# Kernel tuning notes

Measured on AMD Instinct MI355X. Metric: run time of the kernel, lower is better.

Reference implementation:

```python
import jax, jax.numpy as jnp
import numpy as np

BN_EPS = 1e-3  # keras BatchNormalization default epsilon


def batch_norm(x):
    # Fresh keras BatchNorm in training mode: gamma=1, beta=0, batch stats over axis 0
    mean = jnp.mean(x, axis=0, keepdims=True)
    var = jnp.var(x, axis=0, keepdims=True)
    return (x - mean) * jax.lax.rsqrt(var + BN_EPS)


def setup_inputs() -> dict:
    key = jax.random.key(0)
    k1, k2, k3 = jax.random.split(key, 3)
    N, D = 100000, 512
    x1 = jax.random.normal(k1, (N, D), dtype=jnp.float32)
    x2 = jax.random.normal(k2, (N, D), dtype=jnp.float32)
    # glorot_uniform for [D, D] kernel
    limit = np.sqrt(6.0 / (D + D)).astype(np.float32)
    kernel = jax.random.uniform(k3, (D, D), dtype=jnp.float32, minval=-limit, maxval=limit)
    return {"x1": x1, "x2": x2, "kernel": kernel}


def reference(x1, x2, kernel):
    b1 = batch_norm(x1)  # [N, D]
    b2 = batch_norm(x2)  # [N, D]
    gate = jax.nn.relu(jnp.tanh(b1 @ kernel))  # [N, D]; dropout_rate=0 -> no dropout
    out = jnp.tanh(b2 * (1.0 - gate) + b1 * gate)
    return out
```

## Files before the change

kernel.cpp:

```cpp
#include <hip/hip_runtime.h>
#include <hip/hip_fp16.h>
#include <stdint.h>

#define N_ROWS 100000
#define DCOLS 512
#define BN_EPS 1e-3f
#define PB 256

typedef __attribute__((ext_vector_type(8))) _Float16 f16x8;
typedef __attribute__((ext_vector_type(4))) float f32x4;
typedef __attribute__((ext_vector_type(4))) unsigned short u16x4;
typedef __attribute__((ext_vector_type(4))) unsigned int u32x4;

__device__ inline float fast_tanh(float x) {
  float e = __expf(2.0f * x);
  return 1.0f - 2.0f * __builtin_amdgcn_rcpf(e + 1.0f);
}
__device__ inline void gld16(const void* g, void* l) {
  __builtin_amdgcn_global_load_lds(
      (const __attribute__((address_space(1))) void*)g,
      (__attribute__((address_space(3))) void*)l, 16, 0, 0);
}
__device__ inline unsigned int h2u(__half2 h) {
  unsigned int u;
  __builtin_memcpy(&u, &h, 4);
  return u;
}
__device__ inline f16x8 u2f(const u32x4& u) {
  f16x8 h;
  __builtin_memcpy(&h, &u, 16);
  return h;
}

__device__ inline void split8h(const float4& v0, const float4& v1,
                               f16x8& hi8, f16x8& lo8) {
  __half2 h0 = __floats2half2_rn(v0.x, v0.y);
  __half2 h1 = __floats2half2_rn(v0.z, v0.w);
  __half2 h2 = __floats2half2_rn(v1.x, v1.y);
  __half2 h3 = __floats2half2_rn(v1.z, v1.w);
  __half2 l0 = __floats2half2_rn(v0.x - __low2float(h0), v0.y - __high2float(h0));
  __half2 l1 = __floats2half2_rn(v0.z - __low2float(h1), v0.w - __high2float(h1));
  __half2 l2 = __floats2half2_rn(v1.x - __low2float(h2), v1.y - __high2float(h2));
  __half2 l3 = __floats2half2_rn(v1.z - __low2float(h3), v1.w - __high2float(h3));
  u32x4 hi = (u32x4){h2u(h0), h2u(h1), h2u(h2), h2u(h3)};
  u32x4 lo = (u32x4){h2u(l0), h2u(l1), h2u(l2), h2u(l3)};
  hi8 = u2f(hi);
  lo8 = u2f(lo);
}

__global__ __launch_bounds__(256) void k_stats_partial(
    const float* __restrict__ x1, const float* __restrict__ x2,
    float* __restrict__ psum, float* __restrict__ psq) {
  const int CH = (N_ROWS + PB - 1) / PB;
  int bx = blockIdx.x;
  int arr = blockIdx.y;
  const float* x = arr ? x2 : x1;
  int r0 = bx * CH;
  int r1 = min(N_ROWS, r0 + CH);
  int c0 = threadIdx.x * 2;
  float s0 = 0.f, s1 = 0.f, q0 = 0.f, q1 = 0.f;
#pragma unroll 8
  for (int r = r0; r < r1; ++r) {
    float2 v = *(const float2*)(x + (size_t)r * DCOLS + c0);
    s0 += v.x; s1 += v.y;
    q0 += v.x * v.x; q1 += v.y * v.y;
  }
  size_t base = ((size_t)(arr * PB + bx)) * DCOLS + c0;
  psum[base] = s0; psum[base + 1] = s1;
  psq[base]  = q0; psq[base + 1]  = q1;
}

__global__ __launch_bounds__(512) void k_stats_final(
    const float* __restrict__ psum, const float* __restrict__ psq,
    float* __restrict__ stats, float* __restrict__ cvec) {
  int a = blockIdx.x;
  int c = threadIdx.x;
  if (a == 0) cvec[c] = 0.f;
  float sa[8], qa[8];
#pragma unroll
  for (int u = 0; u < 8; ++u) { sa[u] = 0.f; qa[u] = 0.f; }
  for (int b = 0; b < PB; b += 8) {
#pragma unroll
    for (int u = 0; u < 8; ++u) {
      size_t base = ((size_t)(a * PB + b + u)) * DCOLS + c;
      sa[u] += psum[base];
      qa[u] += psq[base];
    }
  }
  float s = ((sa[0]+sa[1])+(sa[2]+sa[3]))+((sa[4]+sa[5])+(sa[6]+sa[7]));
  float q = ((qa[0]+qa[1])+(qa[2]+qa[3]))+((qa[4]+qa[5])+(qa[6]+qa[7]));
  float inv = 1.0f / (float)N_ROWS;
  float mean = s * inv;
  float var = q * inv - mean * mean;
  float scale = rsqrtf(var + BN_EPS);
  stats[a * 1024 + c] = scale;
  stats[a * 1024 + 512 + c] = -mean * scale;
}

__global__ __launch_bounds__(256) void k_prepw(
    const float* __restrict__ wk, const float* __restrict__ stats,
    u32x4* __restrict__ wf, float* __restrict__ cvec) {
  int gid = blockIdx.x * 256 + threadIdx.x;
  int j = gid & 511;
  int kg = gid >> 9;
  int k0 = kg * 8;
  const float* negms1 = stats + 512;
  unsigned short h[8];
  float cacc = 0.f;
#pragma unroll
  for (int u = 0; u < 8; ++u) {
    float wr = wk[(size_t)(k0 + u) * DCOLS + j];
    cacc += negms1[k0 + u] * wr;
    float w = wr * stats[k0 + u];
    __half hh = __float2half_rn(w);
    h[u] = __half_as_ushort(hh);
  }
  atomicAdd(cvec + j, cacc);
  int slice = k0 >> 5;
  int lr = (k0 >> 3) & 3;
  int lane = (lr << 4) | (j & 15);
  int g = j >> 4;
  int idx = slice * 2048 + g * 64 + lane;
  u16x4* ph = (u16x4*)&wf[idx];
  u16x4 h0 = {h[0], h[1], h[2], h[3]};
  u16x4 h1 = {h[4], h[5], h[6], h[7]};
  ph[0] = h0; ph[1] = h1;
}

__global__ __launch_bounds__(512, 4) void k_main(
    const float* __restrict__ x1, const float* __restrict__ x2,
    const float* __restrict__ stats, const float* __restrict__ cvec,
    const u32x4* __restrict__ wf, float* __restrict__ out) {
  __shared__ char smem[32768];

  const int tid = threadIdx.x;
  const int lane = tid & 63;
  const int wv = tid >> 6;
  const int ra = lane & 15;
  const int rq = lane >> 4;

  const int xcd = blockIdx.x & 7;
  const int wgid = xcd * 391 + (blockIdx.x >> 3);
  const int panel = wgid >> 2;
  const int q = wgid & 3;
  const int row0 = panel * 128;
  const int col0 = q * 128;

  int arow = row0 + wv * 16 + ra;
  arow = min(arow, N_ROWS - 1);
  const float* abase = x1 + (size_t)arow * DCOLS + rq * 8;

  const u32x4* bsrc[2];
  int bdst[2];
#pragma unroll
  for (int e = 0; e < 2; ++e) {
    int id = wv * 2 + e;
    int kk = id >> 3, g = id & 7;
    bsrc[e] = wf + (size_t)kk * 2048 + (size_t)(q * 8 + g) * 64 + lane;
    bdst[e] = id * 1024;
  }

  f32x4 acc[8];
#pragma unroll
  for (int g = 0; g < 8; ++g) {
    float cj = cvec[col0 + g * 16 + ra];
    acc[g] = (f32x4){cj, cj, cj, cj};
  }

  float4 av[2][4];

  auto stageB = [&](int s, int buf) {
#pragma unroll
    for (int e = 0; e < 2; ++e)
      gld16(bsrc[e] + (size_t)s * 2 * 2048, smem + buf * 16384 + bdst[e]);
  };
  auto loadA = [&](int s, int pset) {
    const float* p = abase + s * 64;
    av[pset][0] = *(const float4*)(p);
    av[pset][1] = *(const float4*)(p + 4);
    av[pset][2] = *(const float4*)(p + 32);
    av[pset][3] = *(const float4*)(p + 36);
  };

  stageB(0, 0);
  asm volatile("" ::: "memory");
  loadA(0, 0);
  asm volatile("s_waitcnt vmcnt(4)" ::: "memory");
  __builtin_amdgcn_s_barrier();
  __builtin_amdgcn_sched_barrier(0);

#pragma unroll
  for (int s = 0; s < 8; ++s) {
    const int p = s & 1;
    if (s < 7) {
      stageB(s + 1, p ^ 1);
      asm volatile("" ::: "memory");
      loadA(s + 1, p ^ 1);
      __builtin_amdgcn_sched_barrier(0);
    }
#pragma unroll
    for (int kk = 0; kk < 2; ++kk) {
      f16x8 bf[8];
#pragma unroll
      for (int g = 0; g < 8; ++g)
        bf[g] = *(const f16x8*)(smem + p * 16384 + (kk * 8 + g) * 1024 +
                                lane * 16);
      f16x8 ah, al;
      split8h(av[p][kk * 2], av[p][kk * 2 + 1], ah, al);
      __builtin_amdgcn_s_setprio(1);
#pragma unroll
      for (int g = 0; g < 8; ++g)
        acc[g] = __builtin_amdgcn_mfma_f32_16x16x32_f16(ah, bf[g], acc[g],
                                                        0, 0, 0);
#pragma unroll
      for (int g = 0; g < 8; ++g)
        acc[g] = __builtin_amdgcn_mfma_f32_16x16x32_f16(al, bf[g], acc[g],
                                                        0, 0, 0);
      __builtin_amdgcn_s_setprio(0);
    }
    if (s < 7) {
      asm volatile("s_waitcnt vmcnt(4)" ::: "memory");
      __builtin_amdgcn_s_barrier();
      __builtin_amdgcn_sched_barrier(0);
    }
  }

  const float* scale1 = stats;
  const float* negms1 = stats + 512;
  const float* scale2 = stats + 1024;
  const float* negms2 = stats + 1536;

  float s1j[8], n1j[8], s2j[8], n2j[8];
#pragma unroll
  for (int g = 0; g < 8; ++g) {
    int j = col0 + g * 16 + ra;
    s1j[g] = scale1[j]; n1j[g] = negms1[j];
    s2j[g] = scale2[j]; n2j[g] = negms2[j];
  }
#pragma unroll
  for (int r = 0; r < 4; ++r) {
    int n = row0 + wv * 16 + rq * 4 + r;
    if (n < N_ROWS) {
#pragma unroll
      for (int g = 0; g < 8; ++g) {
        int j = col0 + g * 16 + ra;
        float c = acc[g][r];
        float tt = fast_tanh(c);
        float gt = fmaxf(tt, 0.0f);
        size_t idx = (size_t)n * DCOLS + j;
        float b1v = fmaf(x1[idx], s1j[g], n1j[g]);
        float b2v = fmaf(x2[idx], s2j[g], n2j[g]);
        out[idx] = fast_tanh(b2v + gt * (b1v - b2v));
      }
    }
  }
}

extern "C" void kernel_launch(void* const* d_in, const int* in_sizes, int n_in,
                              void* d_out, int out_size, void* d_ws, size_t ws_size,
                              hipStream_t stream) {
  const float* x1 = (const float*)d_in[0];
  const float* x2 = (const float*)d_in[1];
  const float* wk = (const float*)d_in[2];
  float* out = (float*)d_out;
  char* ws = (char*)d_ws;

  if (ws_size < (size_t)(4u << 20)) return;

  float* psum  = (float*)ws;
  float* psq   = (float*)(ws + (1 << 20));
  float* stats = (float*)(ws + (2 << 20));
  float* cvec  = (float*)(ws + (2 << 20) + (160 << 10));
  u32x4* wf    = (u32x4*)(ws + (3 << 20));

  k_stats_partial<<<dim3(PB, 2), 256, 0, stream>>>(x1, x2, psum, psq);
  k_stats_final<<<2, 512, 0, stream>>>(psum, psq, stats, cvec);
  k_prepw<<<128, 256, 0, stream>>>(wk, stats, wf, cvec);

  const int nblocks = 8 * 391;
  k_main<<<nblocks, 512, 0, stream>>>(x1, x2, stats, cvec, wf, out);
}
```

Before: 299.2 us.

## Double K-stage depth to 128 and split A register loads into halves

The GEMM main loop now stages 128 K-values of the fp16 weight tile per step in a 64KB double-buffered LDS region. That halves the number of stages and barriers. A-operand fp32 loads are split into two register halves, so the second half loads while the first half's MFMAs run. The cost is twice the LDS per block, which likely cuts resident blocks per CU below the launch-bounds target of 4. The mid-stage vmcnt(0) wait also blocks on the next B prefetch, which can reduce overlap.

Result: no change. 295.1 us (-1.4%).

```diff
diff --git a/kernel.cpp b/kernel.cpp
--- a/kernel.cpp
+++ b/kernel.cpp
@@ -131,7 +131,7 @@
     const float* __restrict__ x1, const float* __restrict__ x2,
     const float* __restrict__ stats, const float* __restrict__ cvec,
     const u32x4* __restrict__ wf, float* __restrict__ out) {
-  __shared__ char smem[32768];
+  __shared__ char smem[65536];
 
   const int tid = threadIdx.x;
   const int lane = tid & 63;
@@ -150,13 +150,13 @@
   arow = min(arow, N_ROWS - 1);
   const float* abase = x1 + (size_t)arow * DCOLS + rq * 8;
 
-  const u32x4* bsrc[2];
-  int bdst[2];
-#pragma unroll
-  for (int e = 0; e < 2; ++e) {
-    int id = wv * 2 + e;
-    int kk = id >> 3, g = id & 7;
-    bsrc[e] = wf + (size_t)kk * 2048 + (size_t)(q * 8 + g) * 64 + lane;
+  const u32x4* bsrc[4];
+  int bdst[4];
+#pragma unroll
+  for (int e = 0; e < 4; ++e) {
+    int id = wv * 4 + e;
+    int sl = id >> 3, g = id & 7;
+    bsrc[e] = wf + (size_t)sl * 2048 + (size_t)(q * 8 + g) * 64 + lane;
     bdst[e] = id * 1024;
   }
 
@@ -167,46 +167,31 @@
     acc[g] = (f32x4){cj, cj, cj, cj};
   }
 
-  float4 av[2][4];
+  float4 avA[4], avB[4];
 
   auto stageB = [&](int s, int buf) {
 #pragma unroll
-    for (int e = 0; e < 2; ++e)
-      gld16(bsrc[e] + (size_t)s * 2 * 2048, smem + buf * 16384 + bdst[e]);
+    for (int e = 0; e < 4; ++e)
+      gld16(bsrc[e] + (size_t)s * 8192, smem + buf * 32768 + bdst[e]);
   };
-  auto loadA = [&](int s, int pset) {
-    const float* p = abase + s * 64;
-    av[pset][0] = *(const float4*)(p);
-    av[pset][1] = *(const float4*)(p + 4);
-    av[pset][2] = *(const float4*)(p + 32);
-    av[pset][3] = *(const float4*)(p + 36);
+  auto loadA = [&](int s, int half, float4* av) {
+    const float* p = abase + s * 128 + half * 64;
+    av[0] = *(const float4*)(p);
+    av[1] = *(const float4*)(p + 4);
+    av[2] = *(const float4*)(p + 32);
+    av[3] = *(const float4*)(p + 36);
   };
-
-  stageB(0, 0);
-  asm volatile("" ::: "memory");
-  loadA(0, 0);
-  asm volatile("s_waitcnt vmcnt(4)" ::: "memory");
-  __builtin_amdgcn_s_barrier();
-  __builtin_amdgcn_sched_barrier(0);
-
-#pragma unroll
-  for (int s = 0; s < 8; ++s) {
-    const int p = s & 1;
-    if (s < 7) {
-      stageB(s + 1, p ^ 1);
-      asm volatile("" ::: "memory");
-      loadA(s + 1, p ^ 1);
-      __builtin_amdgcn_sched_barrier(0);
-    }
-#pragma unroll
-    for (int kk = 0; kk < 2; ++kk) {
+  auto computeHalf = [&](int p, int kkbase, const float4* av) {
+#pragma unroll
+    for (int kk2 = 0; kk2 < 2; ++kk2) {
+      int kk = kkbase + kk2;
       f16x8 bf[8];
 #pragma unroll
       for (int g = 0; g < 8; ++g)
-        bf[g] = *(const f16x8*)(smem + p * 16384 + (kk * 8 + g) * 1024 +
+        bf[g] = *(const f16x8*)(smem + p * 32768 + (kk * 8 + g) * 1024 +
                                 lane * 16);
       f16x8 ah, al;
-      split8h(av[p][kk * 2], av[p][kk * 2 + 1], ah, al);
+      split8h(av[kk2 * 2], av[kk2 * 2 + 1], ah, al);
       __builtin_amdgcn_s_setprio(1);
 #pragma unroll
       for (int g = 0; g < 8; ++g)
@@ -218,7 +203,33 @@
                                                         0, 0, 0);
       __builtin_amdgcn_s_setprio(0);
     }
-    if (s < 7) {
+  };
+
+  stageB(0, 0);
+  asm volatile("" ::: "memory");
+  loadA(0, 0, avA);
+  asm volatile("s_waitcnt vmcnt(0)" ::: "memory");
+  __builtin_amdgcn_s_barrier();
+  __builtin_amdgcn_sched_barrier(0);
+
+#pragma unroll
+  for (int s = 0; s < 4; ++s) {
+    const int p = s & 1;
+    if (s < 3) stageB(s + 1, p ^ 1);
+    asm volatile("" ::: "memory");
+    loadA(s, 1, avB);
+    __builtin_amdgcn_sched_barrier(0);
+
+    computeHalf(p, 0, avA);
+
+    asm volatile("s_waitcnt vmcnt(0)" ::: "memory");
+    __builtin_amdgcn_sched_barrier(0);
+    if (s < 3) loadA(s + 1, 0, avA);
+    __builtin_amdgcn_sched_barrier(0);
+
+    computeHalf(p, 2, avB);
+
+    if (s < 3) {
       asm volatile("s_waitcnt vmcnt(4)" ::: "memory");
       __builtin_amdgcn_s_barrier();
       __builtin_amdgcn_sched_barrier(0);
```

## Drop fp16 hi/lo split of A operand and restage loads for higher occupancy

Applied to the files above, without the earlier changes.

The A operand was split into fp16 high and low halves to emulate higher precision, costing two MFMAs per product. That split is removed, so each product uses a single fp16 MFMA, halving matrix work and register use. The A loads are reorganised into half-stage slices with finer vmcnt waits, and launch bounds are raised to allow six waves per SIMD. The trade-off is lower GEMM accuracy, since only a single fp16 rounding of the normalised-input-scaled activations remains. That may or may not stay within tolerance.

Result: slower. 315.8 us (+5.5%).

```diff
diff --git a/kernel.cpp b/kernel.cpp
--- a/kernel.cpp
+++ b/kernel.cpp
@@ -32,20 +32,13 @@
   return h;
 }
 
-__device__ inline void split8h(const float4& v0, const float4& v1,
-                               f16x8& hi8, f16x8& lo8) {
+__device__ inline f16x8 cvt8h(const float4& v0, const float4& v1) {
   __half2 h0 = __floats2half2_rn(v0.x, v0.y);
   __half2 h1 = __floats2half2_rn(v0.z, v0.w);
   __half2 h2 = __floats2half2_rn(v1.x, v1.y);
   __half2 h3 = __floats2half2_rn(v1.z, v1.w);
-  __half2 l0 = __floats2half2_rn(v0.x - __low2float(h0), v0.y - __high2float(h0));
-  __half2 l1 = __floats2half2_rn(v0.z - __low2float(h1), v0.w - __high2float(h1));
-  __half2 l2 = __floats2half2_rn(v1.x - __low2float(h2), v1.y - __high2float(h2));
-  __half2 l3 = __floats2half2_rn(v1.z - __low2float(h3), v1.w - __high2float(h3));
   u32x4 hi = (u32x4){h2u(h0), h2u(h1), h2u(h2), h2u(h3)};
-  u32x4 lo = (u32x4){h2u(l0), h2u(l1), h2u(l2), h2u(l3)};
-  hi8 = u2f(hi);
-  lo8 = u2f(lo);
+  return u2f(hi);
 }
 
 __global__ __launch_bounds__(256) void k_stats_partial(
@@ -127,7 +120,7 @@
   ph[0] = h0; ph[1] = h1;
 }
 
-__global__ __launch_bounds__(512, 4) void k_main(
+__global__ __launch_bounds__(512, 6) void k_main(
     const float* __restrict__ x1, const float* __restrict__ x2,
     const float* __restrict__ stats, const float* __restrict__ cvec,
     const u32x4* __restrict__ wf, float* __restrict__ out) {
@@ -167,59 +160,70 @@
     acc[g] = (f32x4){cj, cj, cj, cj};
   }
 
-  float4 av[2][4];
+  float4 avA[2], avB[2];
 
   auto stageB = [&](int s, int buf) {
 #pragma unroll
     for (int e = 0; e < 2; ++e)
       gld16(bsrc[e] + (size_t)s * 2 * 2048, smem + buf * 16384 + bdst[e]);
   };
-  auto loadA = [&](int s, int pset) {
-    const float* p = abase + s * 64;
-    av[pset][0] = *(const float4*)(p);
-    av[pset][1] = *(const float4*)(p + 4);
-    av[pset][2] = *(const float4*)(p + 32);
-    av[pset][3] = *(const float4*)(p + 36);
+  auto loadA = [&](int s, int kk, float4* av) {
+    const float* p = abase + s * 64 + kk * 32;
+    av[0] = *(const float4*)(p);
+    av[1] = *(const float4*)(p + 4);
+  };
+  auto computeSlice = [&](int p, int kk, const float4* av) {
+    f16x8 ah = cvt8h(av[0], av[1]);
+    f16x8 bf[4];
+#pragma unroll
+    for (int g = 0; g < 4; ++g)
+      bf[g] = *(const f16x8*)(smem + p * 16384 + (kk * 8 + g) * 1024 +
+                              lane * 16);
+    __builtin_amdgcn_s_setprio(1);
+#pragma unroll
+    for (int g = 0; g < 4; ++g)
+      acc[g] = __builtin_amdgcn_mfma_f32_16x16x32_f16(ah, bf[g], acc[g],
+                                                      0, 0, 0);
+    __builtin_amdgcn_s_setprio(0);
+#pragma unroll
+    for (int g = 0; g < 4; ++g)
+      bf[g] = *(const f16x8*)(smem + p * 16384 + (kk * 8 + 4 + g) * 1024 +
+                              lane * 16);
+    __builtin_amdgcn_s_setprio(1);
+#pragma unroll
+    for (int g = 0; g < 4; ++g)
+      acc[4 + g] = __builtin_amdgcn_mfma_f32_16x16x32_f16(ah, bf[g],
+                                                          acc[4 + g], 0, 0, 0);
+    __builtin_amdgcn_s_setprio(0);
   };
 
   stageB(0, 0);
   asm volatile("" ::: "memory");
-  loadA(0, 0);
-  asm volatile("s_waitcnt vmcnt(4)" ::: "memory");
+  loadA(0, 0, avA);
+  asm volatile("s_waitcnt vmcnt(0)" ::: "memory");
   __builtin_amdgcn_s_barrier();
   __builtin_amdgcn_sched_barrier(0);
 
 #pragma unroll
   for (int s = 0; s < 8; ++s) {
     const int p = s & 1;
+    loadA(s, 1, avB);
+    asm volatile("" ::: "memory");
+    if (s < 7) stageB(s + 1, p ^ 1);
+    __builtin_amdgcn_sched_barrier(0);
+
+    asm volatile("s_waitcnt vmcnt(4)" ::: "memory");
+    __builtin_amdgcn_sched_barrier(0);
+    computeSlice(p, 0, avA);
+
+    asm volatile("s_waitcnt vmcnt(2)" ::: "memory");
+    __builtin_amdgcn_sched_barrier(0);
+    if (s < 7) loadA(s + 1, 0, avA);
+    __builtin_amdgcn_sched_barrier(0);
+    computeSlice(p, 1, avB);
+
     if (s < 7) {
-      stageB(s + 1, p ^ 1);
-      asm volatile("" ::: "memory");
-      loadA(s + 1, p ^ 1);
-      __builtin_amdgcn_sched_barrier(0);
-    }
-#pragma unroll
-    for (int kk = 0; kk < 2; ++kk) {
-      f16x8 bf[8];
-#pragma unroll
-      for (int g = 0; g < 8; ++g)
-        bf[g] = *(const f16x8*)(smem + p * 16384 + (kk * 8 + g) * 1024 +
-                                lane * 16);
-      f16x8 ah, al;
-      split8h(av[p][kk * 2], av[p][kk * 2 + 1], ah, al);
-      __builtin_amdgcn_s_setprio(1);
-#pragma unroll
-      for (int g = 0; g < 8; ++g)
-        acc[g] = __builtin_amdgcn_mfma_f32_16x16x32_f16(ah, bf[g], acc[g],
-                                                        0, 0, 0);
-#pragma unroll
-      for (int g = 0; g < 8; ++g)
-        acc[g] = __builtin_amdgcn_mfma_f32_16x16x32_f16(al, bf[g], acc[g],
-                                                        0, 0, 0);
-      __builtin_amdgcn_s_setprio(0);
-    }
-    if (s < 7) {
-      asm volatile("s_waitcnt vmcnt(4)" ::: "memory");
+      asm volatile("s_waitcnt vmcnt(2)" ::: "memory");
       __builtin_amdgcn_s_barrier();
       __builtin_amdgcn_sched_barrier(0);
     }
```
